# Kernel tuning notes

Measured on AMD Instinct MI355X. Metric: run time of the kernel, lower is better.

The kernel has to match this reference:

```python
import jax, jax.numpy as jnp
import numpy as np

B, T, D, UNITS = 32, 8192, 256, 128


def setup_inputs() -> dict:
    key = jax.random.key(0)
    ks = jax.random.split(key, 6)
    s = 0.05
    return {
        "query": jax.random.normal(ks[0], (B, D), dtype=jnp.float32),
        "values": jax.random.normal(ks[1], (B, T, D), dtype=jnp.float32),
        "W1_kernel": jax.random.normal(ks[2], (D, UNITS), dtype=jnp.float32) * s,
        "W1_bias": jnp.zeros((UNITS,), dtype=jnp.float32),
        "W2_kernel": jax.random.normal(ks[3], (D, UNITS), dtype=jnp.float32) * s,
        "W2_bias": jnp.zeros((UNITS,), dtype=jnp.float32),
        "V_kernel": jax.random.normal(ks[4], (UNITS, 1), dtype=jnp.float32) * s,
        "V_bias": jnp.zeros((1,), dtype=jnp.float32),
    }


def reference(query, values, W1_kernel, W1_bias, W2_kernel, W2_bias, V_kernel, V_bias):
    # W1(values): Dense with relu over last dim -> [B, T, U]
    h_v = jax.nn.relu(jnp.einsum('btd,du->btu', values, W1_kernel) + W1_bias)
    # W2(query) with time axis expanded -> [B, 1, U]
    h_q = jax.nn.relu(query @ W2_kernel + W2_bias)[:, None, :]
    # V(tanh(...)) -> score [B, T, 1]
    score = jnp.tanh(h_v + h_q) @ V_kernel + V_bias
    # softmax over the time axis
    attention_weights = jax.nn.softmax(score, axis=1)  # [B, T, 1]
    # weighted sum of values over T -> [B, D]
    context_vector = jnp.sum(attention_weights * values, axis=1)
    return context_vector, attention_weights
```

## Files before the change

kernel.cpp:

```cpp
#include <hip/hip_runtime.h>
#include <cmath>


#define B_ 32
#define T_ 8192
#define D_ 256
#define U_ 128
#define NBC_ 32
#define GRP_ 520

typedef float f32x4 __attribute__((ext_vector_type(4)));
typedef short s16x8 __attribute__((ext_vector_type(8)));
typedef __bf16 bf16x8 __attribute__((ext_vector_type(8)));

__device__ __forceinline__ float tanh_fast(float x) {
    float e = __expf(2.f * x);
    return 1.f - 2.f * __builtin_amdgcn_rcpf(e + 1.f);
}

__global__ __launch_bounds__(256) void prep(
    const float* __restrict__ W1, const float* __restrict__ query,
    const float* __restrict__ W2, const float* __restrict__ b2,
    unsigned short* __restrict__ W1h, unsigned short* __restrict__ W1l,
    float* __restrict__ hq)
{
    int blk = blockIdx.x, tid = threadIdx.x;
    if (blk < 128) {
        int idx2 = blk * 256 + tid;
        int k = idx2 >> 7, n = idx2 & 127;
        float wv = W1[idx2];
        int kk = k >> 5, j = k & 7, lg = (k >> 3) & 3;
        int lane = lg * 16 + (n & 15);
        int nn = n >> 4;
        int pos = ((kk * 8 + nn) * 64 + lane) * 8 + j;
        __bf16 hb = (__bf16)wv;
        float hf = (float)hb;
        __bf16 lb = (__bf16)(wv - hf);
        W1h[pos] = __builtin_bit_cast(unsigned short, hb);
        W1l[pos] = __builtin_bit_cast(unsigned short, lb);
    } else {
        __shared__ float hq2[256];
        int b = blk - 128;
        int u = tid & 127, half = tid >> 7;
        float acc = half ? 0.f : b2[u];
        const float* q = query + b * D_ + half * 128;
        const float* w2 = W2 + (half * 128) * U_ + u;
        for (int d = 0; d < 128; ++d)
            acc = fmaf(q[d], w2[d * U_], acc);
        hq2[tid] = acc;
        __syncthreads();
        if (tid < 128) hq[b * U_ + tid] = fmaxf(hq2[tid] + hq2[tid + 128], 0.f);
    }
}

__device__ __forceinline__ void stage_load(
    const float* __restrict__ src, int w, int lane, float4 xr[2][2])
{
#pragma unroll
    for (int p = 0; p < 2; ++p) {
        int tile = w * 2 + p;
        int mt = tile >> 3, kk = tile & 7;
        const float* ptr = src + (mt * 16 + (lane & 15)) * D_ + kk * 32 + (lane >> 4) * 8;
        xr[p][0] = *(const float4*)ptr;
        xr[p][1] = *(const float4*)(ptr + 4);
    }
}

__device__ __forceinline__ void stage_store(
    int w, int lane, const float4 xr[2][2],
    unsigned short* __restrict__ Ah, unsigned short* __restrict__ Al)
{
#pragma unroll
    for (int p = 0; p < 2; ++p) {
        int tile = w * 2 + p;
        int mt = tile >> 3, kk = tile & 7;
        float xs[8] = {xr[p][0].x, xr[p][0].y, xr[p][0].z, xr[p][0].w,
                       xr[p][1].x, xr[p][1].y, xr[p][1].z, xr[p][1].w};
        s16x8 hv, lv;
#pragma unroll
        for (int e = 0; e < 8; ++e) {
            __bf16 hb = (__bf16)xs[e];
            float hf = (float)hb;
            __bf16 lb = (__bf16)(xs[e] - hf);
            hv[e] = __builtin_bit_cast(short, hb);
            lv[e] = __builtin_bit_cast(short, lb);
        }
        int off = (mt * 8 + kk) * GRP_ + lane * 8;
        *(s16x8*)&Ah[off] = hv;
        *(s16x8*)&Al[off] = lv;
    }
}

__global__ __launch_bounds__(512, 2) void score_ctx(
    const float* __restrict__ values,
    const unsigned short* __restrict__ W1h, const unsigned short* __restrict__ W1l,
    const float* __restrict__ hq, const float* __restrict__ b1,
    const float* __restrict__ Vk,
    float* __restrict__ sc_g, float* __restrict__ st_g, float* __restrict__ cp_g)
{
    __shared__ __align__(16) unsigned short AhB[2][16 * GRP_];
    __shared__ __align__(16) unsigned short AlB[2][16 * GRP_];
    __shared__ float scp[8][32];
    __shared__ float cbuf[256];

    const int tid = threadIdx.x;
    const int b = blockIdx.x >> 5;
    const int blkc = blockIdx.x & 31;
    const int lane = tid & 63;
    const int w = tid >> 6;
    const int u0 = lane & 15;

    bf16x8 bfh[8], bfl[8];
#pragma unroll
    for (int kk = 0; kk < 8; ++kk) {
        int boff = ((kk * 8 + w) * 64 + lane) * 8;
        bfh[kk] = __builtin_bit_cast(bf16x8, *(const s16x8*)&W1h[boff]);
        bfl[kk] = __builtin_bit_cast(bf16x8, *(const s16x8*)&W1l[boff]);
    }

    const int u = w * 16 + u0;
    const float b1v = b1[u];
    const float hqv = hq[b * U_ + u];
    const float Vv = Vk[u];

    float l_acc = 0.f;
    float c1 = 0.f;
    const int tb = blkc * 256;
    const float* vblk = values + ((size_t)b * T_ + tb) * D_;

    float4 xr[2][2];
    stage_load(vblk, w, lane, xr);
    stage_store(w, lane, xr, AhB[0], AlB[0]);
    int cur = 0;

#pragma unroll 2
    for (int hh = 0; hh < 8; ++hh) {
        __syncthreads();

        if (hh < 7) stage_load(vblk + (size_t)(hh + 1) * 32 * D_, w, lane, xr);

        const unsigned short* Ah = AhB[cur];
        const unsigned short* Al = AlB[cur];
        f32x4 acc[2];
        acc[0] = (f32x4){0.f, 0.f, 0.f, 0.f};
        acc[1] = (f32x4){0.f, 0.f, 0.f, 0.f};
#pragma unroll
        for (int kk = 0; kk < 8; ++kk) {
#pragma unroll
            for (int mt = 0; mt < 2; ++mt) {
                int aoff = (mt * 8 + kk) * GRP_ + lane * 8;
                bf16x8 ah = __builtin_bit_cast(bf16x8, *(const s16x8*)&Ah[aoff]);
                bf16x8 al = __builtin_bit_cast(bf16x8, *(const s16x8*)&Al[aoff]);
                acc[mt] = __builtin_amdgcn_mfma_f32_16x16x32_bf16(ah, bfh[kk], acc[mt], 0, 0, 0);
                acc[mt] = __builtin_amdgcn_mfma_f32_16x16x32_bf16(ah, bfl[kk], acc[mt], 0, 0, 0);
                acc[mt] = __builtin_amdgcn_mfma_f32_16x16x32_bf16(al, bfh[kk], acc[mt], 0, 0, 0);
            }
        }

#pragma unroll
        for (int mt = 0; mt < 2; ++mt) {
            float p[4];
#pragma unroll
            for (int i = 0; i < 4; ++i) {
                float hpre = fmaxf(acc[mt][i] + b1v, 0.f) + hqv;
                p[i] = tanh_fast(hpre) * Vv;
            }
#pragma unroll
            for (int off = 1; off < 16; off <<= 1)
#pragma unroll
                for (int i = 0; i < 4; ++i) p[i] += __shfl_xor(p[i], off, 16);
            if (u0 == 0) {
                int base = mt * 16 + (lane >> 4) * 4;
#pragma unroll
                for (int i = 0; i < 4; ++i) scp[w][base + i] = p[i];
            }
        }
        __syncthreads();

        {
            int t = lane & 31;
            float s = 0.f;
#pragma unroll
            for (int ww = 0; ww < 8; ++ww) s += scp[ww][t];
            float e = __expf(s);
            if (w == 0 && lane < 32) {
                sc_g[(size_t)b * T_ + tb + hh * 32 + lane] = s;
                float lh = e;
#pragma unroll
                for (int off = 16; off >= 1; off >>= 1)
                    lh += __shfl_xor(lh, off, 32);
                if (lane == 0) l_acc += lh;
            }

            int colr = tid & 255, rh = tid >> 8;
            const float* vcol = vblk + (size_t)(hh * 32 + rh * 16) * D_ + colr;
#pragma unroll
            for (int tl = 0; tl < 16; ++tl)
                c1 = fmaf(__shfl(e, rh * 16 + tl, 64), vcol[(size_t)tl * D_], c1);
        }

        if (hh < 7) stage_store(w, lane, xr, AhB[cur ^ 1], AlB[cur ^ 1]);
        cur ^= 1;
    }

    if (tid >= 256) cbuf[tid - 256] = c1;
    __syncthreads();
    if (tid < 256)
        cp_g[((size_t)(b * NBC_ + blkc)) * D_ + tid] = c1 + cbuf[tid];
    if (tid == 0) st_g[b * NBC_ + blkc] = l_acc;
}

__global__ __launch_bounds__(256) void epilogue(
    const float* __restrict__ sc_g, const float* __restrict__ st_g,
    const float* __restrict__ cp_g, float* __restrict__ out)
{
    __shared__ float invL_s;
    int blk = blockIdx.x, tid = threadIdx.x;
    int b = (blk < 256) ? (blk >> 3) : (blk - 256);

    if (tid < 32) {
        float l = st_g[b * NBC_ + tid];
#pragma unroll
        for (int off = 16; off >= 1; off >>= 1)
            l += __shfl_xor(l, off, 32);
        if (tid == 0) invL_s = 1.f / l;
    }
    __syncthreads();
    float invL = invL_s;

    if (blk < 256) {
        int s8 = blk & 7;
        int t = s8 * 1024 + tid * 4;
        float4 s4 = *(const float4*)&sc_g[(size_t)b * T_ + t];
        float4 r;
        r.x = __expf(s4.x) * invL;
        r.y = __expf(s4.y) * invL;
        r.z = __expf(s4.z) * invL;
        r.w = __expf(s4.w) * invL;
        *(float4*)&out[B_ * D_ + (size_t)b * T_ + t] = r;
    } else {
        float a = 0.f;
        const float* p = cp_g + (size_t)b * NBC_ * D_ + tid;
#pragma unroll 8
        for (int c2 = 0; c2 < NBC_; ++c2)
            a += p[(size_t)c2 * D_];
        out[b * D_ + tid] = a * invL;
    }
}

extern "C" void kernel_launch(void* const* d_in, const int* in_sizes, int n_in,
                              void* d_out, int out_size, void* d_ws, size_t ws_size,
                              hipStream_t stream)
{
    const float* query = (const float*)d_in[0];
    const float* values = (const float*)d_in[1];
    const float* W1 = (const float*)d_in[2];
    const float* b1 = (const float*)d_in[3];
    const float* W2 = (const float*)d_in[4];
    const float* b2 = (const float*)d_in[5];
    const float* Vk = (const float*)d_in[6];
    float* out = (float*)d_out;
    char* ws = (char*)d_ws;

    float* scores = (float*)(ws + 0);
    float* hq     = (float*)(ws + 1048576);
    float* stats  = (float*)(ws + 1064960);
    float* ctxp   = (float*)(ws + 1069056);
    unsigned short* W1h = (unsigned short*)(ws + 2117632);
    unsigned short* W1l = (unsigned short*)(ws + 2183168);

    prep<<<160, 256, 0, stream>>>(W1, query, W2, b2, W1h, W1l, hq);
    score_ctx<<<B_ * NBC_, 512, 0, stream>>>(values, W1h, W1l, hq, b1, Vk,
                                             scores, stats, ctxp);
    epilogue<<<288, 256, 0, stream>>>(scores, stats, ctxp, out);
}
```

Before: 389.6 us.

## Compute context partials from register-staged values instead of re-reading global memory

The context accumulation no longer re-reads each 32-row slice of values from global memory. Instead it reuses the float4 registers already loaded for the bf16 staging: each thread scales its staged elements by the exp-score of its row, reduces across 16 lanes with shuffles, and writes per-wave partials to shared memory, which are summed into the per-column accumulator in the next iteration. This removes a second global read of values per block, at the cost of extra shuffles, more live registers (a copy of the staged values) and a new LDS buffer. The score-row mapping and the softmax-denominator reduction are rearranged across waves 0 and 4 to match the new layout.

```diff
diff --git a/kernel.cpp b/kernel.cpp
--- a/kernel.cpp
+++ b/kernel.cpp
@@ -101,7 +101,8 @@
     __shared__ __align__(16) unsigned short AhB[2][16 * GRP_];
     __shared__ __align__(16) unsigned short AlB[2][16 * GRP_];
     __shared__ float scp[8][32];
-    __shared__ float cbuf[256];
+    __shared__ float ctxp_l[8][64];
+    __shared__ float ltail;
 
     const int tid = threadIdx.x;
     const int b = blockIdx.x >> 5;
@@ -109,6 +110,9 @@
     const int lane = tid & 63;
     const int w = tid >> 6;
     const int u0 = lane & 15;
+    const int g = lane >> 4;
+    const int mt_w = w >> 2;
+    const int trow = mt_w * 16 + u0;
 
     bf16x8 bfh[8], bfl[8];
 #pragma unroll
@@ -123,6 +127,10 @@
     const float hqv = hq[b * U_ + u];
     const float Vv = Vk[u];
 
+    const int kkd = (tid & 255) >> 5;
+    const int w0 = kkd >> 1;
+    const int cidx = (kkd & 1) * 32 + (tid & 31);
+
     float l_acc = 0.f;
     float c1 = 0.f;
     const int tb = blkc * 256;
@@ -137,6 +145,12 @@
     for (int hh = 0; hh < 8; ++hh) {
         __syncthreads();
 
+        if (hh > 0 && tid < 256)
+            c1 += ctxp_l[w0][cidx] + ctxp_l[w0 + 4][cidx];
+
+        float4 xc[2][2];
+        xc[0][0] = xr[0][0]; xc[0][1] = xr[0][1];
+        xc[1][0] = xr[1][0]; xc[1][1] = xr[1][1];
         if (hh < 7) stage_load(vblk + (size_t)(hh + 1) * 32 * D_, w, lane, xr);
 
         const unsigned short* Ah = AhB[cur];
@@ -177,37 +191,45 @@
         }
         __syncthreads();
 
-        {
-            int t = lane & 31;
-            float s = 0.f;
-#pragma unroll
-            for (int ww = 0; ww < 8; ++ww) s += scp[ww][t];
-            float e = __expf(s);
-            if (w == 0 && lane < 32) {
-                sc_g[(size_t)b * T_ + tb + hh * 32 + lane] = s;
-                float lh = e;
-#pragma unroll
-                for (int off = 16; off >= 1; off >>= 1)
-                    lh += __shfl_xor(lh, off, 32);
-                if (lane == 0) l_acc += lh;
-            }
-
-            int colr = tid & 255, rh = tid >> 8;
-            const float* vcol = vblk + (size_t)(hh * 32 + rh * 16) * D_ + colr;
-#pragma unroll
-            for (int tl = 0; tl < 16; ++tl)
-                c1 = fmaf(__shfl(e, rh * 16 + tl, 64), vcol[(size_t)tl * D_], c1);
+        float s = 0.f;
+#pragma unroll
+        for (int ww = 0; ww < 8; ++ww) s += scp[ww][trow];
+        float e = __expf(s);
+        if ((w == 0 || w == 4) && lane < 16)
+            sc_g[(size_t)b * T_ + tb + hh * 32 + trow] = s;
+        if (w == 0 || w == 4) {
+            float lh = e;
+#pragma unroll
+            for (int off = 1; off < 16; off <<= 1)
+                lh += __shfl_xor(lh, off, 16);
+            if (lane == 0) l_acc += lh;
+        }
+
+#pragma unroll
+        for (int p = 0; p < 2; ++p) {
+            float pj[8] = {e * xc[p][0].x, e * xc[p][0].y, e * xc[p][0].z, e * xc[p][0].w,
+                           e * xc[p][1].x, e * xc[p][1].y, e * xc[p][1].z, e * xc[p][1].w};
+#pragma unroll
+            for (int off = 1; off < 16; off <<= 1)
+#pragma unroll
+                for (int j = 0; j < 8; ++j) pj[j] += __shfl_xor(pj[j], off, 16);
+            if (u0 == 0) {
+#pragma unroll
+                for (int j = 0; j < 8; ++j) ctxp_l[w][p * 32 + g * 8 + j] = pj[j];
+            }
         }
 
         if (hh < 7) stage_store(w, lane, xr, AhB[cur ^ 1], AlB[cur ^ 1]);
         cur ^= 1;
     }
 
-    if (tid >= 256) cbuf[tid - 256] = c1;
+    if (w == 4 && lane == 0) ltail = l_acc;
     __syncthreads();
-    if (tid < 256)
-        cp_g[((size_t)(b * NBC_ + blkc)) * D_ + tid] = c1 + cbuf[tid];
-    if (tid == 0) st_g[b * NBC_ + blkc] = l_acc;
+    if (tid < 256) {
+        c1 += ctxp_l[w0][cidx] + ctxp_l[w0 + 4][cidx];
+        cp_g[((size_t)(b * NBC_ + blkc)) * D_ + tid] = c1;
+    }
+    if (tid == 0) st_g[b * NBC_ + blkc] = l_acc + ltail;
 }
 
 __global__ __launch_bounds__(256) void epilogue(
```

Measured after the change: 422.3 us. 1.08x slower.
